# Performance work log

Hardware: AMD Instinct MI355X
Metric: run time of the kernel (lower is better)

## Reference

```python
import jax, jax.numpy as jnp
import numpy as np

B, N, S, C, NS = 2, 20000, 1024, 256, 16
RADIUS, HMIN, HMAX = 0.05, -0.02, 0.04
NA, ND = 12, 4
EPS = 1e-5  # BatchNorm eps


def setup_inputs() -> dict:
    key = jax.random.key(0)
    ks = jax.random.split(key, 40)
    def rn(k, shape, scale=0.05):
        return jax.random.normal(k, shape, jnp.float32) * scale
    inp = {
        "xyz": jax.random.uniform(ks[0], (B, N, 3), jnp.float32),
        "new_xyz": jax.random.uniform(ks[1], (B, S, 3), jnp.float32),
        "view_rot": jax.random.normal(ks[2], (B, S, 3, 3), jnp.float32),
        "features": jax.random.normal(ks[3], (B, C, N), jnp.float32),
    }
    i = 4
    for li, (o, ci) in enumerate([(512, C + 3), (256, 512), (256, 256)], 1):
        inp[f"mlp{li}_w"] = rn(ks[i], (o, ci)); inp[f"mlp{li}_b"] = rn(ks[i + 1], (o,))
        inp[f"mlp{li}_g"] = jnp.ones((o,), jnp.float32) + rn(ks[i + 2], (o,), 0.01)
        inp[f"mlp{li}_be"] = rn(ks[i + 3], (o,)); i += 4
    for name in ("c1", "c2"):
        inp[f"{name}_w"] = rn(ks[i], (256, 256)); inp[f"{name}_b"] = rn(ks[i + 1], (256,))
        inp[f"{name}_g"] = jnp.ones((256,), jnp.float32) + rn(ks[i + 2], (256,), 0.01)
        inp[f"{name}_be"] = rn(ks[i + 3], (256,)); i += 4
    inp["c3_w"] = rn(ks[i], (NA * ND * 2, 256)); inp["c3_b"] = rn(ks[i + 1], (NA * ND * 2,))
    return inp


def _bn(x, g, be):  # eval-mode BatchNorm with running_mean=0, running_var=1
    return x * (g / jnp.sqrt(1.0 + EPS)) + be


def _forward(xyz, new_xyz, view_rot, features,
             mlp1_w, mlp1_b, mlp1_g, mlp1_be,
             mlp2_w, mlp2_b, mlp2_g, mlp2_be,
             mlp3_w, mlp3_b, mlp3_g, mlp3_be,
             c1_w, c1_b, c1_g, c1_be,
             c2_w, c2_b, c2_g, c2_be,
             c3_w, c3_b):
    # ---- cylinder query (CUDA kernel math: r = rot @ (p - c), cylinder axis = x) ----
    # computed per rotation row to keep intermediates at (B,S,N) each
    comp = []
    for i in range(3):
        rw = view_rot[:, :, i, :]  # (B,S,3)
        comp.append(jnp.einsum('bsj,bpj->bsp', rw, xyz) - jnp.sum(rw * new_xyz, -1)[..., None])
    xr, yr, zr = comp  # each (B,S,N)
    mask = (yr * yr + zr * zr < RADIUS * RADIUS) & (xr > HMIN) & (xr < HMAX)
    # first-NS valid indices per seed (ascending), pad with first valid (0 if none)
    vals = jnp.where(mask, jnp.arange(N, dtype=jnp.int32), N)  # (B,S,N)
    neg_top, _ = jax.lax.top_k(-vals, NS)
    idx = -neg_top  # (B,S,NS) ascending
    first = idx[..., :1]
    first = jnp.where(first >= N, 0, first)
    idx = jnp.where(idx >= N, first, idx)
    # ---- group ----
    b_ix = jnp.arange(B)[:, None, None]
    g_xyz = xyz[b_ix, idx]                                  # (B,S,NS,3)
    g_feat = jnp.transpose(features, (0, 2, 1))[b_ix, idx]  # (B,S,NS,C)
    diff = (g_xyz - new_xyz[:, :, None, :]) / RADIUS        # normalize_xyz
    rot_xyz = jnp.einsum('bsnk,bskj->bsnj', diff, view_rot)  # rotate_xyz: diff @ rot
    h = jnp.concatenate([rot_xyz, g_feat], axis=-1)          # (B,S,NS,C+3)
    # ---- SharedMLP (1x1 conv2d + BN + ReLU) ----
    for w, bb, g, be in ((mlp1_w, mlp1_b, mlp1_g, mlp1_be),
                         (mlp2_w, mlp2_b, mlp2_g, mlp2_be),
                         (mlp3_w, mlp3_b, mlp3_g, mlp3_be)):
        h = jax.nn.relu(_bn(jnp.einsum('bsnc,oc->bsno', h, w) + bb, g, be))
    h = h.max(axis=2)  # max-pool over samples -> (B,S,256)
    # ---- pointwise conv1d head ----
    h = jax.nn.relu(_bn(jnp.einsum('bsc,oc->bso', h, c1_w) + c1_b, c1_g, c1_be))
    h = jax.nn.relu(_bn(jnp.einsum('bsc,oc->bso', h, c2_w) + c2_b, c2_g, c2_be))
    out = jnp.einsum('bsc,oc->bso', h, c3_w) + c3_b  # (B,S,NA*ND*2)
    return out


def reference(xyz, new_xyz, view_rot, features,
              mlp1_w, mlp1_b, mlp1_g, mlp1_be,
              mlp2_w, mlp2_b, mlp2_g, mlp2_be,
              mlp3_w, mlp3_b, mlp3_g, mlp3_be,
              c1_w, c1_b, c1_g, c1_be,
              c2_w, c2_b, c2_g, c2_be,
              c3_w, c3_b):
    return _forward(xyz, new_xyz, view_rot, features,
                    mlp1_w, mlp1_b, mlp1_g, mlp1_be,
                    mlp2_w, mlp2_b, mlp2_g, mlp2_be,
                    mlp3_w, mlp3_b, mlp3_g, mlp3_be,
                    c1_w, c1_b, c1_g, c1_be,
                    c2_w, c2_b, c2_g, c2_be,
                    c3_w, c3_b)
```

## Files before the change

kernel.cpp:

```cpp
#include <hip/hip_runtime.h>
#include <hip/hip_bf16.h>
#include <stdint.h>
#include <limits.h>

#define B_   2
#define N_   20000
#define S_   1024
#define C_   256
#define NS_  16
#define NQ   (B_ * S_)
#define M_   (NQ * NS_)
#define K1P  288
#define O1   512
#define O2   256
#define O3   256
#define OUTC 96

#define R2C   ((float)(0.05 * 0.05))
#define HMINC ((float)(-0.02))
#define HMAXC ((float)(0.04))

#define GDIM   16
#define GCELLS (GDIM * GDIM * GDIM)
#define GTOT   (B_ * GCELLS)
#define CAP    256

__device__ __forceinline__ unsigned short f2b(float f) {
    union { float f; unsigned int i; } x; x.f = f;
    unsigned int r = x.i + 0x7FFFu + ((x.i >> 16) & 1u);
    return (unsigned short)(r >> 16);
}
__device__ __forceinline__ float b2f(unsigned short u) {
    union { unsigned int i; float f; } x; x.i = ((unsigned int)u) << 16; return x.f;
}

__global__ __launch_bounds__(256) void prep_w123(const float* __restrict__ m1w,
                                                 const float* __restrict__ m2w,
                                                 const float* __restrict__ m3w,
                                                 unsigned short* __restrict__ w1p,
                                                 unsigned short* __restrict__ w2p,
                                                 unsigned short* __restrict__ w3p) {
    int i = blockIdx.x * 256 + threadIdx.x;
    if (i < O1 * K1P) {
        int o = i / K1P, k = i - o * K1P;
        float v = 0.0f;
        if (k < 256)      v = m1w[o * 259 + 3 + k];
        else if (k < 259) v = m1w[o * 259 + (k - 256)];
        w1p[i] = (k < 259) ? f2b(v) : (unsigned short)0;
    } else if (i < O1 * K1P + O2 * 512) {
        int j = i - O1 * K1P;
        w2p[j] = f2b(m2w[j]);
    } else if (i < O1 * K1P + O2 * 512 + O3 * 256) {
        int j = i - O1 * K1P - O2 * 512;
        w3p[j] = f2b(m3w[j]);
    }
}

__global__ __launch_bounds__(256) void prep_head_w(const float* __restrict__ c1w,
                                                   const float* __restrict__ c2w,
                                                   const float* __restrict__ c3w,
                                                   unsigned short* __restrict__ c1wb,
                                                   unsigned short* __restrict__ c2wb,
                                                   unsigned short* __restrict__ c3wb) {
    int i = blockIdx.x * 256 + threadIdx.x;
    if (i < 65536) {
        c1wb[i] = f2b(c1w[i]);
    } else if (i < 131072) {
        c2wb[i - 65536] = f2b(c2w[i - 65536]);
    } else if (i < 163840) {
        int j = i - 131072;
        int o = j >> 8, k = j & 255;
        c3wb[j] = (o < OUTC) ? f2b(c3w[o * 256 + k]) : (unsigned short)0;
    }
}

__global__ __launch_bounds__(256) void transpose_feat(const float* __restrict__ feat,
                                                      unsigned short* __restrict__ feat_t) {
    __shared__ float tile[32][33];
    int n0 = blockIdx.x * 32, c0 = blockIdx.y * 32, b = blockIdx.z;
    int t = threadIdx.x;
    int nl = t & 31;
#pragma unroll
    for (int i = 0; i < 4; ++i) {
        int cl = (t >> 5) + i * 8;
        tile[cl][nl] = feat[((size_t)(b * C_ + c0 + cl)) * N_ + n0 + nl];
    }
    __syncthreads();
    int nr = t >> 3, c4 = (t & 7) * 4;
    ushort4 v;
    v.x = f2b(tile[c4 + 0][nr]);
    v.y = f2b(tile[c4 + 1][nr]);
    v.z = f2b(tile[c4 + 2][nr]);
    v.w = f2b(tile[c4 + 3][nr]);
    *(ushort4*)(feat_t + ((size_t)(b * N_ + n0 + nr)) * C_ + c0 + c4) = v;
}

__global__ __launch_bounds__(256) void grid_zero(int* __restrict__ c) {
    c[blockIdx.x * 256 + threadIdx.x] = 0;
}

__device__ __forceinline__ int cell_of(float px, float py, float pz, int b) {
    int cx = (int)(px * (float)GDIM); cx = min(GDIM - 1, max(0, cx));
    int cy = (int)(py * (float)GDIM); cy = min(GDIM - 1, max(0, cy));
    int cz = (int)(pz * (float)GDIM); cz = min(GDIM - 1, max(0, cz));
    return b * GCELLS + cz * (GDIM * GDIM) + cy * GDIM + cx;
}

__global__ __launch_bounds__(256) void grid_count(const float* __restrict__ xyz,
                                                  int* __restrict__ counts) {
    int i = blockIdx.x * 256 + threadIdx.x;
    if (i < B_ * N_) {
        int b = i / N_;
        const float* p = xyz + (size_t)i * 3;
        atomicAdd(counts + cell_of(p[0], p[1], p[2], b), 1);
    }
}

__global__ __launch_bounds__(256) void grid_scan(const int* __restrict__ counts,
                                                 int* __restrict__ start,
                                                 int* __restrict__ cursor) {
    __shared__ int part[256];
    int t = threadIdx.x;
    int local[32];
    int s = 0;
#pragma unroll
    for (int i = 0; i < 32; ++i) { local[i] = counts[t * 32 + i]; s += local[i]; }
    part[t] = s;
    __syncthreads();
    if (t == 0) {
        int r = 0;
        for (int i = 0; i < 256; ++i) { int x = part[i]; part[i] = r; r += x; }
    }
    __syncthreads();
    int r = part[t];
#pragma unroll
    for (int i = 0; i < 32; ++i) {
        start[t * 32 + i] = r;
        cursor[t * 32 + i] = r;
        r += local[i];
    }
    if (t == 255) start[GTOT] = r;
}

__global__ __launch_bounds__(256) void grid_scatter(const float* __restrict__ xyz,
                                                    int* __restrict__ cursor,
                                                    float4* __restrict__ sorted) {
    int i = blockIdx.x * 256 + threadIdx.x;
    if (i < B_ * N_) {
        int b = i / N_, n = i - b * N_;
        const float* p = xyz + (size_t)i * 3;
        float px = p[0], py = p[1], pz = p[2];
        int pos = atomicAdd(cursor + cell_of(px, py, pz, b), 1);
        sorted[pos] = make_float4(px, py, pz, __int_as_float(n));
    }
}

__device__ __forceinline__ void sort16(int* buf, int cnt, int lane) {
    asm volatile("s_waitcnt lgkmcnt(0)" ::: "memory");
    __builtin_amdgcn_sched_barrier(0);
    int a0 = INT_MAX, a1 = INT_MAX, a2 = INT_MAX, a3 = INT_MAX;
    if (lane < cnt)       a0 = buf[lane];
    if (lane + 64 < cnt)  a1 = buf[lane + 64];
    if (lane + 128 < cnt) a2 = buf[lane + 128];
    if (lane + 192 < cnt) a3 = buf[lane + 192];
#pragma unroll
    for (int t = 0; t < NS_; ++t) {
        int v = a0, sl = 0;
        if (a1 < v) { v = a1; sl = 1; }
        if (a2 < v) { v = a2; sl = 2; }
        if (a3 < v) { v = a3; sl = 3; }
        int pp = (sl << 6) | lane;
#pragma unroll
        for (int off = 1; off < 64; off <<= 1) {
            int ov = __shfl_xor(v, off);
            int op = __shfl_xor(pp, off);
            if (ov < v) { v = ov; pp = op; }
        }
        if ((pp & 63) == lane) {
            int s = pp >> 6;
            if (s == 0) a0 = INT_MAX;
            else if (s == 1) a1 = INT_MAX;
            else if (s == 2) a2 = INT_MAX;
            else a3 = INT_MAX;
        }
        if (lane == 0) buf[t] = v;
    }
    asm volatile("s_waitcnt lgkmcnt(0)" ::: "memory");
    __builtin_amdgcn_sched_barrier(0);
}

#define SCAN_SPAN(SS, EE)                                                    \
    for (int base = (SS); base < (EE); base += 64) {                         \
        int p = base + lane;                                                 \
        bool m = false; int n = 0;                                           \
        if (p < (EE)) {                                                      \
            float4 v = sorted[p];                                            \
            n = __float_as_int(v.w);                                         \
            float px = v.x, py = v.y, pz = v.z;                              \
            float xr = ((R[0]*px + R[1]*py) + R[2]*pz) - dq0;                \
            float yr = ((R[3]*px + R[4]*py) + R[5]*pz) - dq1;                \
            float zr = ((R[6]*px + R[7]*py) + R[8]*pz) - dq2;                \
            m = ((yr*yr + zr*zr) < R2C) && (xr > HMINC) && (xr < HMAXC);     \
        }                                                                    \
        unsigned long long bal = __ballot(m);                                \
        if (m) {                                                             \
            int pos = cnt + __popcll(bal & ((1ull << lane) - 1ull));         \
            buf[pos] = n;                                                    \
        }                                                                    \
        int h = __popcll(bal);                                               \
        cnt += h; tot += h;                                                  \
        if (cnt > CAP - 64) { sort16(buf, cnt, lane); cnt = NS_; }           \
    }

__global__ __launch_bounds__(256) void cyl_query_grid(const float* __restrict__ new_xyz,
                                                      const float* __restrict__ view_rot,
                                                      const float4* __restrict__ sorted,
                                                      const int* __restrict__ cell_start,
                                                      int* __restrict__ idx_out) {
#pragma clang fp contract(off)
    int w = threadIdx.x >> 6, lane = threadIdx.x & 63;
    int q = blockIdx.x;
    int b = q >> 10;

    __shared__ int bufs[4][CAP];
    __shared__ int tots[4];
    int* buf = bufs[w];

    const float* nq = new_xyz + (size_t)q * 3;
    float qx = nq[0], qy = nq[1], qz = nq[2];
    const float* rp = view_rot + (size_t)q * 9;
    float R[9];
#pragma unroll
    for (int i = 0; i < 9; ++i) R[i] = rp[i];
    float dq0 = (R[0]*qx + R[1]*qy) + R[2]*qz;
    float dq1 = (R[3]*qx + R[4]*qy) + R[5]*qz;
    float dq2 = (R[6]*qx + R[7]*qy) + R[8]*qz;

    int x0 = 0, x1 = GDIM - 1, y0 = 0, y1 = GDIM - 1, z0 = 0, z1 = GDIM - 1;
    bool ok = false;
    {
        float det = R[0]*(R[4]*R[8]-R[5]*R[7])
                  - R[1]*(R[3]*R[8]-R[5]*R[6])
                  + R[2]*(R[3]*R[7]-R[4]*R[6]);
        float adet = fabsf(det);
        if (adet > 1e-30f) {
            ok = true;
            float id = 1.0f / det;
            float m00 = (R[4]*R[8]-R[5]*R[7])*id, m01 = (R[2]*R[7]-R[1]*R[8])*id, m02 = (R[1]*R[5]-R[2]*R[4])*id;
            float m10 = (R[5]*R[6]-R[3]*R[8])*id, m11 = (R[0]*R[8]-R[2]*R[6])*id, m12 = (R[2]*R[3]-R[0]*R[5])*id;
            float m20 = (R[3]*R[7]-R[4]*R[6])*id, m21 = (R[1]*R[6]-R[0]*R[7])*id, m22 = (R[0]*R[4]-R[1]*R[3])*id;
            const float mid = 0.5f * (HMINC + HMAXC);
            const float hh  = 0.5f * (HMAXC - HMINC);
            float cx = qx + m00 * mid, cy = qy + m10 * mid, cz = qz + m20 * mid;
            float ex = hh * fabsf(m00) + 0.05f * sqrtf(m01*m01 + m02*m02);
            float ey = hh * fabsf(m10) + 0.05f * sqrtf(m11*m11 + m12*m12);
            float ez = hh * fabsf(m20) + 0.05f * sqrtf(m21*m21 + m22*m22);
            ex = ex * 1.002f + 1e-3f;
            ey = ey * 1.002f + 1e-3f;
            ez = ez * 1.002f + 1e-3f;
            x0 = (int)fmaxf(0.0f, fminf((float)(GDIM - 1), floorf((cx - ex) * (float)GDIM)));
            x1 = (int)fmaxf(0.0f, fminf((float)(GDIM - 1), floorf((cx + ex) * (float)GDIM)));
            y0 = (int)fmaxf(0.0f, fminf((float)(GDIM - 1), floorf((cy - ey) * (float)GDIM)));
            y1 = (int)fmaxf(0.0f, fminf((float)(GDIM - 1), floorf((cy + ey) * (float)GDIM)));
            z0 = (int)fmaxf(0.0f, fminf((float)(GDIM - 1), floorf((cz - ez) * (float)GDIM)));
            z1 = (int)fmaxf(0.0f, fminf((float)(GDIM - 1), floorf((cz + ez) * (float)GDIM)));
        }
    }

    int nx = x1 - x0 + 1, ny = y1 - y0 + 1, nz = z1 - z0 + 1;
    bool heavy = (!ok) || (ny * nz > 256) || (nx * ny * nz > 512);

    int cnt = 0, tot = 0;
    int cbase = b * GCELLS;

    if (!heavy) {
        int NR = ny * nz;
        int nr_w = (NR - w + 3) >> 2;
        int sl = 0, el = 0;
        if (lane < nr_w) {
            int ri = w + (lane << 2);
            int zi = ri / ny;
            int yi = ri - zi * ny;
            int cid = cbase + (z0 + zi) * (GDIM * GDIM) + (y0 + yi) * GDIM;
            sl = cell_start[cid + x0];
            el = cell_start[cid + x1 + 1];
        }
        for (int j = 0; j < nr_w; ++j) {
            int s = __shfl(sl, j), e = __shfl(el, j);
            SCAN_SPAN(s, e)
        }
    } else {
        int bstart = b * N_;
        int per = (N_ + 3) >> 2;
        int s = bstart + w * per;
        int e = min(bstart + N_, s + per);
        SCAN_SPAN(s, e)
    }

    sort16(buf, cnt, lane);
    if (lane == 0) tots[w] = tot;
    __syncthreads();

    if (w == 0) {
        int cand = bufs[lane >> 4][lane & 15];
        int myv = INT_MAX;
#pragma unroll
        for (int t = 0; t < NS_; ++t) {
            int v = cand, pp = lane;
#pragma unroll
            for (int off = 1; off < 64; off <<= 1) {
                int ov = __shfl_xor(v, off);
                int op = __shfl_xor(pp, off);
                if (ov < v) { v = ov; pp = op; }
            }
            if (lane == t) myv = v;
            if (pp == lane) cand = INT_MAX;
        }
        int tt = tots[0] + tots[1] + tots[2] + tots[3];
        int total = tt < NS_ ? tt : NS_;
        int first = (tt > 0) ? __shfl(myv, 0) : 0;
        if (lane < NS_)
            idx_out[q * NS_ + lane] = (lane < total) ? myv : first;
    }
}

__global__ __launch_bounds__(256) void build_h0(const float* __restrict__ xyz,
                                                const float* __restrict__ new_xyz,
                                                const float* __restrict__ view_rot,
                                                const unsigned short* __restrict__ feat_t,
                                                const int* __restrict__ idxs,
                                                unsigned short* __restrict__ h0) {
#pragma clang fp contract(off)
    int q = blockIdx.x;
    int b = q >> 10;
    int t = threadIdx.x;
    __shared__ int pidx[NS_];
    if (t < NS_) pidx[t] = idxs[q * NS_ + t];
    __syncthreads();

#pragma unroll
    for (int pass = 0; pass < 2; ++pass) {
        int n = pass * 8 + (t >> 5);
        int p = pidx[n];
        uint4 v = *(const uint4*)(feat_t + ((size_t)(b * N_ + p)) * C_ + (t & 31) * 8);
        *(uint4*)(h0 + (size_t)(q * NS_ + n) * K1P + (t & 31) * 8) = v;
    }

    if (t < NS_) {
        int n = t, p = pidx[n];
        const float* pp = xyz + ((size_t)b * N_ + p) * 3;
        const float* nq = new_xyz + (size_t)q * 3;
        float dx = (pp[0] - nq[0]) / 0.05f;
        float dy = (pp[1] - nq[1]) / 0.05f;
        float dz = (pp[2] - nq[2]) / 0.05f;
        const float* rp = view_rot + (size_t)q * 9;
        float r0 = (dx * rp[0] + dy * rp[3]) + dz * rp[6];
        float r1 = (dx * rp[1] + dy * rp[4]) + dz * rp[7];
        float r2 = (dx * rp[2] + dy * rp[5]) + dz * rp[8];
        size_t row = (size_t)(q * NS_ + n) * K1P;
        h0[row + 256] = f2b(r0);
        h0[row + 257] = f2b(r1);
        h0[row + 258] = f2b(r2);
    }
    for (int e = t; e < NS_ * 29; e += 256) {
        int n = e / 29, c = 259 + (e - n * 29);
        h0[(size_t)(q * NS_ + n) * K1P + c] = 0;
    }
}

typedef float f32x4 __attribute__((ext_vector_type(4)));
typedef short s16x8 __attribute__((ext_vector_type(8)));

__global__ __launch_bounds__(256) void gemm_bn_relu(const unsigned short* __restrict__ A,
                                                    const unsigned short* __restrict__ W,
                                                    const float* __restrict__ bias,
                                                    const float* __restrict__ gam,
                                                    const float* __restrict__ bet,
                                                    unsigned short* __restrict__ out,
                                                    int M, int Nn, int K) {
    __shared__ __align__(16) unsigned short As[128 * 32];
    __shared__ __align__(16) unsigned short Bs[128 * 32];
    int tid  = threadIdx.x;
    int lane = tid & 63, wave = tid >> 6;
    int m0 = blockIdx.x * 128, n0 = blockIdx.y * 128;
    int wm = (wave >> 1) * 64, wn = (wave & 1) * 64;

    f32x4 acc[4][4] = {};

    for (int k0 = 0; k0 < K; k0 += 32) {
        __syncthreads();
#pragma unroll
        for (int j = 0; j < 2; ++j) {
            int e = j * 256 + tid;
            int r = e >> 2, c8 = (e & 3) << 3;
            *(uint4*)&As[e * 8] = *(const uint4*)(A + (size_t)(m0 + r) * K + k0 + c8);
            *(uint4*)&Bs[e * 8] = *(const uint4*)(W + (size_t)(n0 + r) * K + k0 + c8);
        }
        __syncthreads();

        int kq = (lane >> 4) * 8, rr = lane & 15;
        s16x8 af[4], bfr[4];
#pragma unroll
        for (int i = 0; i < 4; ++i) af[i]  = *(const s16x8*)&As[(wm + i * 16 + rr) * 32 + kq];
#pragma unroll
        for (int j = 0; j < 4; ++j) bfr[j] = *(const s16x8*)&Bs[(wn + j * 16 + rr) * 32 + kq];
#pragma unroll
        for (int i = 0; i < 4; ++i)
#pragma unroll
            for (int j = 0; j < 4; ++j)
                acc[i][j] = __builtin_amdgcn_mfma_f32_16x16x32_bf16(af[i], bfr[j], acc[i][j], 0, 0, 0);
    }

    float inv = 1.0f / sqrtf(1.0f + 1e-5f);
    int col = lane & 15, rq = (lane >> 4) * 4;
#pragma unroll
    for (int j = 0; j < 4; ++j) {
        int n = n0 + wn + j * 16 + col;
        float sc = gam[n] * inv;
        float tb = bias[n] * sc + bet[n];
#pragma unroll
        for (int i = 0; i < 4; ++i) {
            int mbase = m0 + wm + i * 16 + rq;
#pragma unroll
            for (int r = 0; r < 4; ++r) {
                float v = acc[i][j][r] * sc + tb;
                v = fmaxf(v, 0.0f);
                out[(size_t)(mbase + r) * Nn + n] = f2b(v);
            }
        }
    }
}

__global__ __launch_bounds__(256) void gemm_bn_relu_maxpool(const unsigned short* __restrict__ A,
                                                            const unsigned short* __restrict__ W,
                                                            const float* __restrict__ bias,
                                                            const float* __restrict__ gam,
                                                            const float* __restrict__ bet,
                                                            unsigned short* __restrict__ hp,
                                                            int M, int Nn, int K) {
    __shared__ __align__(16) unsigned short As[128 * 32];
    __shared__ __align__(16) unsigned short Bs[128 * 32];
    int tid  = threadIdx.x;
    int lane = tid & 63, wave = tid >> 6;
    int m0 = blockIdx.x * 128, n0 = blockIdx.y * 128;
    int wm = (wave >> 1) * 64, wn = (wave & 1) * 64;

    f32x4 acc[4][4] = {};

    for (int k0 = 0; k0 < K; k0 += 32) {
        __syncthreads();
#pragma unroll
        for (int j = 0; j < 2; ++j) {
            int e = j * 256 + tid;
            int r = e >> 2, c8 = (e & 3) << 3;
            *(uint4*)&As[e * 8] = *(const uint4*)(A + (size_t)(m0 + r) * K + k0 + c8);
            *(uint4*)&Bs[e * 8] = *(const uint4*)(W + (size_t)(n0 + r) * K + k0 + c8);
        }
        __syncthreads();

        int kq = (lane >> 4) * 8, rr = lane & 15;
        s16x8 af[4], bfr[4];
#pragma unroll
        for (int i = 0; i < 4; ++i) af[i]  = *(const s16x8*)&As[(wm + i * 16 + rr) * 32 + kq];
#pragma unroll
        for (int j = 0; j < 4; ++j) bfr[j] = *(const s16x8*)&Bs[(wn + j * 16 + rr) * 32 + kq];
#pragma unroll
        for (int i = 0; i < 4; ++i)
#pragma unroll
            for (int j = 0; j < 4; ++j)
                acc[i][j] = __builtin_amdgcn_mfma_f32_16x16x32_bf16(af[i], bfr[j], acc[i][j], 0, 0, 0);
    }

    float inv = 1.0f / sqrtf(1.0f + 1e-5f);
    int col = lane & 15;
    int qbase = (m0 + wm) >> 4;
#pragma unroll
    for (int j = 0; j < 4; ++j) {
        int n = n0 + wn + j * 16 + col;
        float sc = gam[n] * inv;
        float tb = bias[n] * sc + bet[n];
#pragma unroll
        for (int i = 0; i < 4; ++i) {
            float mx = 0.0f;
#pragma unroll
            for (int r = 0; r < 4; ++r)
                mx = fmaxf(mx, acc[i][j][r] * sc + tb);
            mx = fmaxf(mx, __shfl_xor(mx, 16, 64));
            mx = fmaxf(mx, __shfl_xor(mx, 32, 64));
            if (lane < 16)
                hp[(size_t)(qbase + i) * Nn + n] = f2b(mx);
        }
    }
}

__global__ __launch_bounds__(256) void gemm_c3(const unsigned short* __restrict__ A,
                                               const unsigned short* __restrict__ W,
                                               const float* __restrict__ bias,
                                               float* __restrict__ out,
                                               int M, int K) {
    __shared__ __align__(16) unsigned short As[128 * 32];
    __shared__ __align__(16) unsigned short Bs[128 * 32];
    int tid  = threadIdx.x;
    int lane = tid & 63, wave = tid >> 6;
    int m0 = blockIdx.x * 128;
    int wm = (wave >> 1) * 64, wn = (wave & 1) * 64;

    f32x4 acc[4][4] = {};

    for (int k0 = 0; k0 < K; k0 += 32) {
        __syncthreads();
#pragma unroll
        for (int j = 0; j < 2; ++j) {
            int e = j * 256 + tid;
            int r = e >> 2, c8 = (e & 3) << 3;
            *(uint4*)&As[e * 8] = *(const uint4*)(A + (size_t)(m0 + r) * K + k0 + c8);
            *(uint4*)&Bs[e * 8] = *(const uint4*)(W + (size_t)r * K + k0 + c8);
        }
        __syncthreads();

        int kq = (lane >> 4) * 8, rr = lane & 15;
        s16x8 af[4], bfr[4];
#pragma unroll
        for (int i = 0; i < 4; ++i) af[i]  = *(const s16x8*)&As[(wm + i * 16 + rr) * 32 + kq];
#pragma unroll
        for (int j = 0; j < 4; ++j) bfr[j] = *(const s16x8*)&Bs[(wn + j * 16 + rr) * 32 + kq];
#pragma unroll
        for (int i = 0; i < 4; ++i)
#pragma unroll
            for (int j = 0; j < 4; ++j)
                acc[i][j] = __builtin_amdgcn_mfma_f32_16x16x32_bf16(af[i], bfr[j], acc[i][j], 0, 0, 0);
    }

    int col = lane & 15, rq = (lane >> 4) * 4;
#pragma unroll
    for (int j = 0; j < 4; ++j) {
        int n = wn + j * 16 + col;
        if (n >= OUTC) continue;
        float bb = bias[n];
#pragma unroll
        for (int i = 0; i < 4; ++i) {
            int mbase = m0 + wm + i * 16 + rq;
#pragma unroll
            for (int r = 0; r < 4; ++r)
                out[(size_t)(mbase + r) * OUTC + n] = acc[i][j][r] + bb;
        }
    }
}

extern "C" void kernel_launch(void* const* d_in, const int* in_sizes, int n_in,
                              void* d_out, int out_size, void* d_ws, size_t ws_size,
                              hipStream_t stream) {
    const float* xyz      = (const float*)d_in[0];
    const float* new_xyz  = (const float*)d_in[1];
    const float* view_rot = (const float*)d_in[2];
    const float* feat     = (const float*)d_in[3];
    const float* m1w = (const float*)d_in[4];
    const float* m1b = (const float*)d_in[5];
    const float* m1g = (const float*)d_in[6];
    const float* m1be= (const float*)d_in[7];
    const float* m2w = (const float*)d_in[8];
    const float* m2b = (const float*)d_in[9];
    const float* m2g = (const float*)d_in[10];
    const float* m2be= (const float*)d_in[11];
    const float* m3w = (const float*)d_in[12];
    const float* m3b = (const float*)d_in[13];
    const float* m3g = (const float*)d_in[14];
    const float* m3be= (const float*)d_in[15];
    const float* c1w = (const float*)d_in[16];
    const float* c1b = (const float*)d_in[17];
    const float* c1g = (const float*)d_in[18];
    const float* c1be= (const float*)d_in[19];
    const float* c2w = (const float*)d_in[20];
    const float* c2b = (const float*)d_in[21];
    const float* c2g = (const float*)d_in[22];
    const float* c2be= (const float*)d_in[23];
    const float* c3w = (const float*)d_in[24];
    const float* c3b = (const float*)d_in[25];

    char* ws = (char*)d_ws;
    int*            idxs = (int*)ws;
    unsigned short* w1p  = (unsigned short*)(ws + 131072);
    unsigned short* w2p  = (unsigned short*)(ws + 425984);
    unsigned short* w3p  = (unsigned short*)(ws + 688128);
    unsigned short* h0   = (unsigned short*)(ws + 819200);
    char*           h1b  = ws + 19693568;
    unsigned short* h1   = (unsigned short*)h1b;
    unsigned short* h2   = h0;
    unsigned short* featt= (unsigned short*)(h1b + 12582912);
    unsigned short* hp   = (unsigned short*)(h1b + 0);
    unsigned short* g1   = (unsigned short*)(h1b + 4194304);
    unsigned short* g2   = (unsigned short*)(h1b + 8388608);
    unsigned short* c1wb = (unsigned short*)(h1b + 12582912);
    unsigned short* c2wb = (unsigned short*)(h1b + 13631488);
    unsigned short* c3wb = (unsigned short*)(h1b + 14680064);
    float4*         srt  = (float4*)(h1b + 0);
    int*            gcnt = (int*)(h1b + 640000);
    int*            gsta = (int*)(h1b + 672768);
    int*            gcur = (int*)(h1b + 705552);

    hipLaunchKernelGGL(prep_w123, dim3((O1 * K1P + O2 * 512 + O3 * 256) / 256), dim3(256), 0, stream,
                       m1w, m2w, m3w, w1p, w2p, w3p);
    hipLaunchKernelGGL(grid_zero, dim3(GTOT / 256), dim3(256), 0, stream, gcnt);
    hipLaunchKernelGGL(grid_count, dim3((B_ * N_ + 255) / 256), dim3(256), 0, stream, xyz, gcnt);
    hipLaunchKernelGGL(grid_scan, dim3(1), dim3(256), 0, stream, gcnt, gsta, gcur);
    hipLaunchKernelGGL(grid_scatter, dim3((B_ * N_ + 255) / 256), dim3(256), 0, stream, xyz, gcur, srt);
    hipLaunchKernelGGL(cyl_query_grid, dim3(NQ), dim3(256), 0, stream,
                       new_xyz, view_rot, srt, gsta, idxs);
    hipLaunchKernelGGL(transpose_feat, dim3(N_ / 32, C_ / 32, B_), dim3(256), 0, stream, feat, featt);
    hipLaunchKernelGGL(build_h0, dim3(NQ), dim3(256), 0, stream, xyz, new_xyz, view_rot, featt, idxs, h0);
    hipLaunchKernelGGL(gemm_bn_relu, dim3(M_ / 128, O1 / 128), dim3(256), 0, stream,
                       h0, w1p, m1b, m1g, m1be, h1, M_, O1, K1P);
    hipLaunchKernelGGL(gemm_bn_relu, dim3(M_ / 128, O2 / 128), dim3(256), 0, stream,
                       h1, w2p, m2b, m2g, m2be, h2, M_, O2, 512);
    hipLaunchKernelGGL(prep_head_w, dim3(163840 / 256), dim3(256), 0, stream,
                       c1w, c2w, c3w, c1wb, c2wb, c3wb);
    hipLaunchKernelGGL(gemm_bn_relu_maxpool, dim3(M_ / 128, O3 / 128), dim3(256), 0, stream,
                       h2, w3p, m3b, m3g, m3be, hp, M_, O3, 256);
    hipLaunchKernelGGL(gemm_bn_relu, dim3(NQ / 128, 256 / 128), dim3(256), 0, stream,
                       hp, c1wb, c1b, c1g, c1be, g1, NQ, 256, 256);
    hipLaunchKernelGGL(gemm_bn_relu, dim3(NQ / 128, 256 / 128), dim3(256), 0, stream,
                       g1, c2wb, c2b, c2g, c2be, g2, NQ, 256, 256);
    hipLaunchKernelGGL(gemm_c3, dim3(NQ / 128), dim3(256), 0, stream,
                       g2, c3wb, c3b, (float*)d_out, NQ, 256);
}
```

Baseline: 286.7 us.

## Split heavy cylinder queries into chunked multi-block scans with a merge kernel

Queries whose cylinder bounding box covers too many grid cells were scanned over all N points by a single 4-wave block. They are now compacted into a list through an atomic counter, then each is split into 8 chunks of 2500 points handled by separate blocks, with a merge kernel selecting the first 16 indices. The goal is to remove long-tail blocks that serialize the query kernel. In exchange it adds two kernel launches and extra workspace traffic, and the new blocks mostly exit early when few queries are heavy.

```diff
diff --git a/kernel.cpp b/kernel.cpp
--- a/kernel.cpp
+++ b/kernel.cpp
@@ -24,6 +24,8 @@
 #define GCELLS (GDIM * GDIM * GDIM)
 #define GTOT   (B_ * GCELLS)
 #define CAP    256
+#define HCH    8
+#define HPTS   2500
 
 __device__ __forceinline__ unsigned short f2b(float f) {
     union { float f; unsigned int i; } x; x.f = f;
@@ -95,8 +97,9 @@
     *(ushort4*)(feat_t + ((size_t)(b * N_ + n0 + nr)) * C_ + c0 + c4) = v;
 }
 
-__global__ __launch_bounds__(256) void grid_zero(int* __restrict__ c) {
+__global__ __launch_bounds__(256) void grid_zero(int* __restrict__ c, int* __restrict__ hc) {
     c[blockIdx.x * 256 + threadIdx.x] = 0;
+    if (blockIdx.x == 0 && threadIdx.x == 0) *hc = 0;
 }
 
 __device__ __forceinline__ int cell_of(float px, float py, float pz, int b) {
@@ -216,6 +219,8 @@
                                                       const float* __restrict__ view_rot,
                                                       const float4* __restrict__ sorted,
                                                       const int* __restrict__ cell_start,
+                                                      int* __restrict__ hvy_cnt,
+                                                      int* __restrict__ hvy_list,
                                                       int* __restrict__ idx_out) {
 #pragma clang fp contract(off)
     int w = threadIdx.x >> 6, lane = threadIdx.x & 63;
@@ -270,10 +275,18 @@
     int nx = x1 - x0 + 1, ny = y1 - y0 + 1, nz = z1 - z0 + 1;
     bool heavy = (!ok) || (ny * nz > 256) || (nx * ny * nz > 512);
 
+    if (heavy) {
+        if (threadIdx.x == 0) {
+            int s = atomicAdd(hvy_cnt, 1);
+            hvy_list[s] = q;
+        }
+        return;
+    }
+
     int cnt = 0, tot = 0;
     int cbase = b * GCELLS;
 
-    if (!heavy) {
+    {
         int NR = ny * nz;
         int nr_w = (NR - w + 3) >> 2;
         int sl = 0, el = 0;
@@ -289,12 +302,6 @@
             int s = __shfl(sl, j), e = __shfl(el, j);
             SCAN_SPAN(s, e)
         }
-    } else {
-        int bstart = b * N_;
-        int per = (N_ + 3) >> 2;
-        int s = bstart + w * per;
-        int e = min(bstart + N_, s + per);
-        SCAN_SPAN(s, e)
     }
 
     sort16(buf, cnt, lane);
@@ -322,6 +329,108 @@
         if (lane < NS_)
             idx_out[q * NS_ + lane] = (lane < total) ? myv : first;
     }
+}
+
+__global__ __launch_bounds__(256) void cyl_heavy_scan(const float* __restrict__ new_xyz,
+                                                      const float* __restrict__ view_rot,
+                                                      const float4* __restrict__ sorted,
+                                                      const int* __restrict__ hvy_cnt,
+                                                      const int* __restrict__ hvy_list,
+                                                      int* __restrict__ hvy_res) {
+#pragma clang fp contract(off)
+    int w = threadIdx.x >> 6, lane = threadIdx.x & 63;
+    __shared__ int bufs[4][CAP];
+    __shared__ int tots[4];
+    int* buf = bufs[w];
+
+    int hc = *hvy_cnt;
+    int items = hc * HCH;
+    for (int item = blockIdx.x; item < items; item += NQ) {
+        int slot = item >> 3, chunk = item & (HCH - 1);
+        int q = hvy_list[slot];
+        int b = q >> 10;
+
+        const float* nq = new_xyz + (size_t)q * 3;
+        float qx = nq[0], qy = nq[1], qz = nq[2];
+        const float* rp = view_rot + (size_t)q * 9;
+        float R[9];
+#pragma unroll
+        for (int i = 0; i < 9; ++i) R[i] = rp[i];
+        float dq0 = (R[0]*qx + R[1]*qy) + R[2]*qz;
+        float dq1 = (R[3]*qx + R[4]*qy) + R[5]*qz;
+        float dq2 = (R[6]*qx + R[7]*qy) + R[8]*qz;
+
+        int s0 = b * N_ + chunk * HPTS;
+        int ws0 = s0 + w * (HPTS / 4);
+        int we0 = ws0 + (HPTS / 4);
+
+        int cnt = 0, tot = 0;
+        SCAN_SPAN(ws0, we0)
+
+        sort16(buf, cnt, lane);
+        if (lane == 0) tots[w] = tot;
+        __syncthreads();
+
+        if (w == 0) {
+            int cand = bufs[lane >> 4][lane & 15];
+            int myv = INT_MAX;
+#pragma unroll
+            for (int t = 0; t < NS_; ++t) {
+                int v = cand, pp = lane;
+#pragma unroll
+                for (int off = 1; off < 64; off <<= 1) {
+                    int ov = __shfl_xor(v, off);
+                    int op = __shfl_xor(pp, off);
+                    if (ov < v) { v = ov; pp = op; }
+                }
+                if (lane == t) myv = v;
+                if (pp == lane) cand = INT_MAX;
+            }
+            int tt = tots[0] + tots[1] + tots[2] + tots[3];
+            int* dst = hvy_res + (size_t)(slot * HCH + chunk) * 17;
+            if (lane < NS_) dst[lane] = myv;
+            if (lane == 0) dst[16] = tt;
+        }
+        __syncthreads();
+    }
+}
+
+__global__ __launch_bounds__(64) void cyl_heavy_merge(const int* __restrict__ hvy_cnt,
+                                                      const int* __restrict__ hvy_list,
+                                                      const int* __restrict__ hvy_res,
+                                                      int* __restrict__ idx_out) {
+    int slot = blockIdx.x;
+    if (slot >= *hvy_cnt) return;
+    int lane = threadIdx.x;
+    int q = hvy_list[slot];
+    const int* base = hvy_res + (size_t)slot * (HCH * 17);
+    int a0 = base[(lane >> 4) * 17 + (lane & 15)];
+    int a1 = base[(4 + (lane >> 4)) * 17 + (lane & 15)];
+    int tot = 0;
+#pragma unroll
+    for (int c = 0; c < HCH; ++c) tot += base[c * 17 + 16];
+
+    int myv = INT_MAX;
+#pragma unroll
+    for (int t = 0; t < NS_; ++t) {
+        int v = a0, sl = 0;
+        if (a1 < v) { v = a1; sl = 1; }
+        int pp = (sl << 6) | lane;
+#pragma unroll
+        for (int off = 1; off < 64; off <<= 1) {
+            int ov = __shfl_xor(v, off);
+            int op = __shfl_xor(pp, off);
+            if (ov < v) { v = ov; pp = op; }
+        }
+        if ((pp & 63) == lane) {
+            if (pp >> 6) a1 = INT_MAX; else a0 = INT_MAX;
+        }
+        if (lane == t) myv = v;
+    }
+    int total = tot < NS_ ? tot : NS_;
+    int first = (tot > 0) ? __shfl(myv, 0) : 0;
+    if (lane < NS_)
+        idx_out[q * NS_ + lane] = (lane < total) ? myv : first;
 }
 
 __global__ __launch_bounds__(256) void build_h0(const float* __restrict__ xyz,
@@ -597,15 +706,22 @@
     int*            gcnt = (int*)(h1b + 640000);
     int*            gsta = (int*)(h1b + 672768);
     int*            gcur = (int*)(h1b + 705552);
+    int*            hcnt = (int*)(h1b + 738320);
+    int*            hlst = (int*)(h1b + 738336);
+    int*            hres = (int*)(h1b + 746528);
 
     hipLaunchKernelGGL(prep_w123, dim3((O1 * K1P + O2 * 512 + O3 * 256) / 256), dim3(256), 0, stream,
                        m1w, m2w, m3w, w1p, w2p, w3p);
-    hipLaunchKernelGGL(grid_zero, dim3(GTOT / 256), dim3(256), 0, stream, gcnt);
+    hipLaunchKernelGGL(grid_zero, dim3(GTOT / 256), dim3(256), 0, stream, gcnt, hcnt);
     hipLaunchKernelGGL(grid_count, dim3((B_ * N_ + 255) / 256), dim3(256), 0, stream, xyz, gcnt);
     hipLaunchKernelGGL(grid_scan, dim3(1), dim3(256), 0, stream, gcnt, gsta, gcur);
     hipLaunchKernelGGL(grid_scatter, dim3((B_ * N_ + 255) / 256), dim3(256), 0, stream, xyz, gcur, srt);
     hipLaunchKernelGGL(cyl_query_grid, dim3(NQ), dim3(256), 0, stream,
-                       new_xyz, view_rot, srt, gsta, idxs);
+                       new_xyz, view_rot, srt, gsta, hcnt, hlst, idxs);
+    hipLaunchKernelGGL(cyl_heavy_scan, dim3(NQ), dim3(256), 0, stream,
+                       new_xyz, view_rot, srt, hcnt, hlst, hres);
+    hipLaunchKernelGGL(cyl_heavy_merge, dim3(NQ), dim3(64), 0, stream,
+                       hcnt, hlst, hres, idxs);
     hipLaunchKernelGGL(transpose_feat, dim3(N_ / 32, C_ / 32, B_), dim3(256), 0, stream, feat, featt);
     hipLaunchKernelGGL(build_h0, dim3(NQ), dim3(256), 0, stream, xyz, new_xyz, view_rot, featt, idxs, h0);
     hipLaunchKernelGGL(gemm_bn_relu, dim3(M_ / 128, O1 / 128), dim3(256), 0, stream,
```

Result: slower. 308.5 us (+7.6%).
